# Kernel optimization log

Measured on AMD Instinct MI355X. Metric: run time of the kernel, lower is better.

The kernel has to match this reference:

```python
import math
import jax, jax.numpy as jnp
import numpy as np

N_HEADS = 16
D_EMBED = 1024
D_HEAD = D_EMBED // N_HEADS
BATCH = 2
SEQ = 2048


def setup_inputs() -> dict:
    key = jax.random.key(0)
    k1, k2, k3 = jax.random.split(key, 3)
    scale = 1.0 / math.sqrt(D_EMBED)
    return {
        "x": jax.random.normal(k1, (1, BATCH, SEQ, D_EMBED), dtype=jnp.float32),
        "w_in": jax.random.normal(k2, (3 * D_EMBED, D_EMBED), dtype=jnp.float32) * scale,
        "b_in": jnp.zeros((3 * D_EMBED,), dtype=jnp.float32),
        "w_out": jax.random.normal(k3, (D_EMBED, D_EMBED), dtype=jnp.float32) * scale,
        "b_out": jnp.zeros((D_EMBED,), dtype=jnp.float32),
        "causal_mask": 1,
    }


def reference(x, w_in, b_in, w_out, b_out, causal_mask):
    lead, B, S, D = x.shape  # lead == 1
    H, dh = N_HEADS, D_HEAD
    # fused QKV projection (torch Linear: x @ W^T + b)
    qkv = jnp.einsum("lbsd,ed->lbse", x, w_in) + b_in
    q, k, v = jnp.split(qkv, 3, axis=-1)
    # [1,B,S,D] -> [B,H,S,dh]
    def to_heads(t):
        return t.reshape(B, S, H, dh).transpose(0, 2, 1, 3)
    q, k, v = to_heads(q), to_heads(k), to_heads(v)
    # scaled dot-product attention with optional causal mask
    scores = jnp.einsum("bhqd,bhkd->bhqk", q, k)
    if causal_mask:
        mask = jnp.triu(jnp.ones((S, S), dtype=bool), k=1)
        scores = jnp.where(mask, -jnp.inf, scores)
    scores = scores / math.sqrt(dh)
    attn = jax.nn.softmax(scores, axis=-1)
    out = jnp.einsum("bhqk,bhkd->bhqd", attn, v)
    out = out.transpose(0, 2, 1, 3).reshape(lead, B, S, D)
    return jnp.einsum("lbsd,ed->lbse", out, w_out) + b_out
```

## Files before the change

kernel.cpp:

```cpp
#include <hip/hip_runtime.h>
#include <hip/hip_bf16.h>
#include <stdint.h>

#define S_LEN 2048
#define D_EMB 1024
#define NHEAD 16
#define DHEAD 64
#define NBATCH 2
#define MROWS 4096

typedef __attribute__((ext_vector_type(8))) short bf16x8;
typedef __attribute__((ext_vector_type(4))) float f32x4;
typedef unsigned short u16;
typedef unsigned int u32;

__device__ __forceinline__ u16 f2bf(float f) {
  union { float f; u32 u; } v; v.f = f;
  u32 r = v.u + 0x7fffu + ((v.u >> 16) & 1u);
  return (u16)(r >> 16);
}

__device__ __forceinline__ void gl_lds16(const void* g, void* l) {
  __builtin_amdgcn_global_load_lds(
      (const __attribute__((address_space(1))) u32*)g,
      (__attribute__((address_space(3))) u32*)l, 16, 0, 0);
}

__device__ __forceinline__ int swz(int o) { return o ^ (((o >> 7) & 7) << 4); }

__global__ void cast_f32_bf16(const float* __restrict__ in, u16* __restrict__ out, int n4) {
  int i = blockIdx.x * blockDim.x + threadIdx.x;
  if (i < n4) {
    float4 v = reinterpret_cast<const float4*>(in)[i];
    ushort4 o;
    o.x = f2bf(v.x); o.y = f2bf(v.y); o.z = f2bf(v.z); o.w = f2bf(v.w);
    reinterpret_cast<ushort4*>(out)[i] = o;
  }
}

template <int EPI>
__launch_bounds__(256, 2)
__global__ void gemm_bt(const u16* __restrict__ A, const u16* __restrict__ Bm,
                        const float* __restrict__ bias, int M, int N, int K,
                        u16* __restrict__ q_out, u16* __restrict__ k_out,
                        u16* __restrict__ vt_out, float* __restrict__ f_out) {
  __shared__ __align__(16) u16 As[2][128 * 32];
  __shared__ __align__(16) u16 Bs[2][128 * 32];
  const int t = threadIdx.x;
  const int w = t >> 6, lane = t & 63;
  const int m0 = blockIdx.y * 128, n0 = blockIdx.x * 128;
  const int wr = w >> 1, wc = w & 1;

  f32x4 acc[4][4] = {};

  const int e0 = w * 512 + lane * 8;
  const int ar0 = e0 >> 5, ac0 = e0 & 31;
  const int e1 = e0 + 2048;
  const int ar1 = e1 >> 5, ac1 = e1 & 31;
  const u16* Ab0 = A + (size_t)(m0 + ar0) * K + ac0;
  const u16* Ab1 = A + (size_t)(m0 + ar1) * K + ac1;
  const u16* Bb0 = Bm + (size_t)(n0 + ar0) * K + ac0;
  const u16* Bb1 = Bm + (size_t)(n0 + ar1) * K + ac1;

  const int lr = lane & 15, lg = lane >> 4;

#define GSTAGE(KT, BUF)                                \
  do {                                                 \
    gl_lds16(Ab0 + (KT), &As[BUF][w * 512]);           \
    gl_lds16(Ab1 + (KT), &As[BUF][w * 512 + 2048]);    \
    gl_lds16(Bb0 + (KT), &Bs[BUF][w * 512]);           \
    gl_lds16(Bb1 + (KT), &Bs[BUF][w * 512 + 2048]);    \
  } while (0)

  GSTAGE(0, 0);
  __syncthreads();
  int cur = 0;
  for (int kt = 0; kt < K; kt += 32) {
    if (kt + 32 < K) GSTAGE(kt + 32, cur ^ 1);
    bf16x8 af[4], bfr[4];
#pragma unroll
    for (int i = 0; i < 4; i++)
      af[i] = *(const bf16x8*)&As[cur][(wr * 64 + i * 16 + lr) * 32 + lg * 8];
#pragma unroll
    for (int j = 0; j < 4; j++)
      bfr[j] = *(const bf16x8*)&Bs[cur][(wc * 64 + j * 16 + lr) * 32 + lg * 8];
#pragma unroll
    for (int i = 0; i < 4; i++)
#pragma unroll
      for (int j = 0; j < 4; j++)
        acc[i][j] = __builtin_amdgcn_mfma_f32_16x16x32_bf16(af[i], bfr[j], acc[i][j], 0, 0, 0);
    __syncthreads();
    cur ^= 1;
  }
#undef GSTAGE

#pragma unroll
  for (int j = 0; j < 4; j++) {
    const int n = n0 + wc * 64 + j * 16 + lr;
    const float bv = bias[n];
#pragma unroll
    for (int i = 0; i < 4; i++) {
#pragma unroll
      for (int r = 0; r < 4; r++) {
        const int m = m0 + wr * 64 + i * 16 + lg * 4 + r;
        float v = acc[i][j][r] + bv;
        if (EPI == 0) {
          const int which = n >> 10, nn = n & 1023;
          const int h = nn >> 6, d = nn & 63;
          const int b = m >> 11, s = m & 2047;
          if (which == 0)
            q_out[(size_t)(((b * NHEAD + h) * S_LEN) + s) * DHEAD + d] = f2bf(v * 0.180336880f);
          else if (which == 1)
            k_out[(size_t)(((b * NHEAD + h) * S_LEN) + s) * DHEAD + d] = f2bf(v);
          else
            vt_out[(size_t)(((b * NHEAD + h) * DHEAD) + d) * S_LEN + s] = f2bf(v);
        } else {
          f_out[(size_t)m * N + n] = v;
        }
      }
    }
  }
}

__launch_bounds__(512, 2)
__global__ void attn_kernel(const u16* __restrict__ Qg, const u16* __restrict__ Kg,
                            const u16* __restrict__ Vtg, u16* __restrict__ AO,
                            const int* __restrict__ causal) {
  __shared__ __align__(16) u16 Kt[2][64 * 64];
  __shared__ __align__(16) u16 Vt[2][64 * 64];
  __shared__ __align__(16) u16 Pl[8][16 * 72];

  const int t = threadIdx.x, w = t >> 6, lane = t & 63;
  const int lr = lane & 15, lg = lane >> 4;
  const int nqt = (int)gridDim.x;
  const int qt = ((int)blockIdx.y < 16) ? (nqt - 1 - (int)blockIdx.x) : (int)blockIdx.x;
  const int bh = blockIdx.y;
  const size_t bh_off = (size_t)bh * S_LEN * DHEAD;
  const int cz = *causal;
  const int q0 = qt * 128;
  const int nk = cz ? (2 * qt + 2) : (S_LEN / 64);

  bf16x8 ones;
#pragma unroll
  for (int e = 0; e < 8; e++) ones[e] = (short)16256;

  {
    const char* qb = (const char*)(Qg + bh_off + (size_t)q0 * DHEAD);
#pragma unroll
    for (int c = 0; c < 2; c++) {
      int drel = c * 8192 + w * 1024 + lane * 16;
      gl_lds16(qb + swz(drel), (char*)&Kt[0][0] + c * 8192 + w * 1024);
    }
  }
  __syncthreads();
  bf16x8 qf[2];
#pragma unroll
  for (int ks = 0; ks < 2; ks++) {
    int rq = w * 16 + lr;
    qf[ks] = *(const bf16x8*)((const char*)&Kt[0][0] + swz(rq * 128 + ks * 64 + lg * 16));
  }
  __syncthreads();

  auto stageK = [&](int kt, int buf) {
    const char* kb = (const char*)(Kg + bh_off + (size_t)kt * 64 * DHEAD);
    int drel = w * 1024 + lane * 16;
    gl_lds16(kb + swz(drel), (char*)&Kt[buf][0] + w * 1024);
  };
  auto stageV = [&](int kt, int buf) {
    int drel = w * 1024 + lane * 16;
    int o = swz(drel);
    int row = o >> 7, colb = o & 127;
    const char* vb = (const char*)Vtg +
                     (((size_t)bh * DHEAD + row) * S_LEN + (size_t)kt * 64) * 2 + colb;
    gl_lds16(vb, (char*)&Vt[buf][0] + w * 1024);
  };

  float m_run[4], l_run[4];
  f32x4 o_acc[4] = {};
#pragma unroll
  for (int r = 0; r < 4; r++) { m_run[r] = -INFINITY; l_run[r] = 0.f; }

  stageK(0, 0);
  stageV(0, 0);
  __syncthreads();
  int cur = 0;

  for (int kt = 0; kt < nk; kt++) {
    if (kt + 1 < nk) {
      stageK(kt + 1, cur ^ 1);
      stageV(kt + 1, cur ^ 1);
    }

    f32x4 s[4] = {};
#pragma unroll
    for (int nf = 0; nf < 4; nf++) {
#pragma unroll
      for (int ks = 0; ks < 2; ks++) {
        int r = nf * 16 + lr;
        bf16x8 kf = *(const bf16x8*)((const char*)&Kt[cur][0] + swz(r * 128 + ks * 64 + lg * 16));
        s[nf] = __builtin_amdgcn_mfma_f32_16x16x32_bf16(qf[ks], kf, s[nf], 0, 0, 0);
      }
    }

    if (cz && (kt * 64 + 63 > q0 + w * 16)) {
#pragma unroll
      for (int nf = 0; nf < 4; nf++)
#pragma unroll
        for (int r = 0; r < 4; r++) {
          int kv = kt * 64 + nf * 16 + lr;
          int qr = q0 + w * 16 + lg * 4 + r;
          if (kv > qr) s[nf][r] = -INFINITY;
        }
    }

    float lmax[4];
#pragma unroll
    for (int r = 0; r < 4; r++)
      lmax[r] = fmaxf(fmaxf(s[0][r], s[1][r]), fmaxf(s[2][r], s[3][r]));
    float need = fmaxf(fmaxf(lmax[0] - m_run[0], lmax[1] - m_run[1]),
                       fmaxf(lmax[2] - m_run[2], lmax[3] - m_run[3]));
    if (!__all(need <= 8.0f)) {
      float rmax[4];
#pragma unroll
      for (int r = 0; r < 4; r++) rmax[r] = lmax[r];
#pragma unroll
      for (int mlt = 1; mlt < 16; mlt <<= 1)
#pragma unroll
        for (int r = 0; r < 4; r++) rmax[r] = fmaxf(rmax[r], __shfl_xor(rmax[r], mlt, 64));
#pragma unroll
      for (int r = 0; r < 4; r++) {
        float mn = fmaxf(m_run[r], rmax[r]);
        float scl = exp2f(m_run[r] - mn);
        m_run[r] = mn;
        l_run[r] *= scl;
#pragma unroll
        for (int nf = 0; nf < 4; nf++) o_acc[nf][r] *= scl;
      }
    }

#pragma unroll
    for (int nf = 0; nf < 4; nf++)
#pragma unroll
      for (int r = 0; r < 4; r++) {
        float p = exp2f(s[nf][r] - m_run[r]);
        Pl[w][(lg * 4 + r) * 72 + nf * 16 + lr] = f2bf(p);
      }

    asm volatile("s_waitcnt lgkmcnt(0)" ::: "memory");
    __builtin_amdgcn_sched_barrier(0);

    bf16x8 pf[2];
#pragma unroll
    for (int ks = 0; ks < 2; ks++)
      pf[ks] = *(const bf16x8*)&Pl[w][lr * 72 + ks * 32 + lg * 8];

    f32x4 lsum = {};
    lsum = __builtin_amdgcn_mfma_f32_16x16x32_bf16(pf[0], ones, lsum, 0, 0, 0);
    lsum = __builtin_amdgcn_mfma_f32_16x16x32_bf16(pf[1], ones, lsum, 0, 0, 0);

#pragma unroll
    for (int nf = 0; nf < 4; nf++) {
#pragma unroll
      for (int ks = 0; ks < 2; ks++) {
        int r = nf * 16 + lr;
        bf16x8 vf = *(const bf16x8*)((const char*)&Vt[cur][0] + swz(r * 128 + ks * 64 + lg * 16));
        o_acc[nf] = __builtin_amdgcn_mfma_f32_16x16x32_bf16(pf[ks], vf, o_acc[nf], 0, 0, 0);
      }
    }
#pragma unroll
    for (int r = 0; r < 4; r++) l_run[r] += lsum[r];

    __syncthreads();
    cur ^= 1;
  }

  const int b = bh >> 4, h = bh & 15;
#pragma unroll
  for (int nf = 0; nf < 4; nf++)
#pragma unroll
    for (int r = 0; r < 4; r++) {
      float v = o_acc[nf][r] / l_run[r];
      int qrow = q0 + w * 16 + lg * 4 + r;
      int d = nf * 16 + lr;
      AO[(size_t)(b * S_LEN + qrow) * D_EMB + h * DHEAD + d] = f2bf(v);
    }
}

extern "C" void kernel_launch(void* const* d_in, const int* in_sizes, int n_in,
                              void* d_out, int out_size, void* d_ws, size_t ws_size,
                              hipStream_t stream) {
  const float* x = (const float*)d_in[0];
  const float* w_in = (const float*)d_in[1];
  const float* b_in = (const float*)d_in[2];
  const float* w_out = (const float*)d_in[3];
  const float* b_out = (const float*)d_in[4];
  const int* causal = (const int*)d_in[5];
  float* out = (float*)d_out;

  char* p = (char*)d_ws;
  u16* xb = (u16*)p;  p += (size_t)MROWS * D_EMB * 2;
  u16* wib = (u16*)p; p += (size_t)3 * D_EMB * D_EMB * 2;
  u16* wob = (u16*)p; p += (size_t)D_EMB * D_EMB * 2;
  u16* Qg = (u16*)p;  p += (size_t)MROWS * D_EMB * 2;
  u16* Kg = (u16*)p;  p += (size_t)MROWS * D_EMB * 2;
  u16* Vtg = (u16*)p; p += (size_t)MROWS * D_EMB * 2;
  u16* AO = (u16*)p;  p += (size_t)MROWS * D_EMB * 2;

  {
    int n4 = MROWS * D_EMB / 4;
    cast_f32_bf16<<<(n4 + 255) / 256, 256, 0, stream>>>(x, xb, n4);
  }
  {
    int n4 = 3 * D_EMB * D_EMB / 4;
    cast_f32_bf16<<<(n4 + 255) / 256, 256, 0, stream>>>(w_in, wib, n4);
  }
  {
    int n4 = D_EMB * D_EMB / 4;
    cast_f32_bf16<<<(n4 + 255) / 256, 256, 0, stream>>>(w_out, wob, n4);
  }

  gemm_bt<0><<<dim3(3 * D_EMB / 128, MROWS / 128), 256, 0, stream>>>(
      xb, wib, b_in, MROWS, 3 * D_EMB, D_EMB, Qg, Kg, Vtg, nullptr);

  attn_kernel<<<dim3(S_LEN / 128, NBATCH * NHEAD), 512, 0, stream>>>(Qg, Kg, Vtg, AO, causal);

  gemm_bt<1><<<dim3(D_EMB / 128, MROWS / 128), 256, 0, stream>>>(
      AO, wob, b_out, MROWS, D_EMB, D_EMB, nullptr, nullptr, nullptr, out);
}
```

Baseline: 206.6 us.

## Use 256x256 tile GEMM with 512 threads for QKV projection

Replaces the templated 128x128 GEMM for the QKV projection with a dedicated kernel using 256x256 output tiles, a K-step of 64, 8 waves and swizzled LDS staging via direct global-to-LDS loads. This increases data reuse per LDS load and lowers the global traffic per FLOP. In exchange the grid shrinks to 192 blocks, which leaves some CUs idle, and the larger LDS and register footprint limits occupancy. The output projection keeps the old kernel, now specialised to fp32 output.

```diff
diff --git a/kernel.cpp b/kernel.cpp
--- a/kernel.cpp
+++ b/kernel.cpp
@@ -38,12 +38,91 @@
   }
 }
 
-template <int EPI>
+__launch_bounds__(512, 2)
+__global__ void gemm256_qkv(const u16* __restrict__ A, const u16* __restrict__ Bm,
+                            const float* __restrict__ bias,
+                            u16* __restrict__ q_out, u16* __restrict__ k_out,
+                            u16* __restrict__ vt_out) {
+  __shared__ __align__(16) u16 As[2][256 * 64];
+  __shared__ __align__(16) u16 Bs[2][256 * 64];
+  const int K = 1024;
+  const int t = threadIdx.x, w = t >> 6, lane = t & 63;
+  const int lr = lane & 15, lg = lane >> 4;
+  const int m0 = blockIdx.y * 256, n0 = blockIdx.x * 256;
+  const int wr = w >> 2, wc = w & 3;
+
+  f32x4 acc[8][4] = {};
+
+  const int srow = w * 8 + (lane >> 3);
+  const int scol = ((lane & 7) ^ (lane >> 3)) * 8;
+  const u16* Asrc = A + (size_t)(m0 + srow) * K + scol;
+  const u16* Bsrc = Bm + (size_t)(n0 + srow) * K + scol;
+
+#define STAGE256(KT, BUF)                                                     \
+  do {                                                                        \
+    _Pragma("unroll") for (int c = 0; c < 4; c++) {                           \
+      gl_lds16(Asrc + (size_t)(c * 64) * K + (KT), &As[BUF][c * 4096 + w * 512]); \
+      gl_lds16(Bsrc + (size_t)(c * 64) * K + (KT), &Bs[BUF][c * 4096 + w * 512]); \
+    }                                                                         \
+  } while (0)
+
+  const int xorv = (lane & 7) << 4;
+  const int ofk[2] = {(lg * 16) ^ xorv, (64 + lg * 16) ^ xorv};
+
+  STAGE256(0, 0);
+  __syncthreads();
+  int cur = 0;
+  for (int kt = 0; kt < K; kt += 64) {
+    if (kt + 64 < K) STAGE256(kt + 64, cur ^ 1);
+    const char* Ab = (const char*)&As[cur][0];
+    const char* Bb = (const char*)&Bs[cur][0];
+#pragma unroll
+    for (int ks = 0; ks < 2; ks++) {
+      bf16x8 bfr[4];
+#pragma unroll
+      for (int j = 0; j < 4; j++)
+        bfr[j] = *(const bf16x8*)(Bb + (wc * 64 + j * 16 + lr) * 128 + ofk[ks]);
+#pragma unroll
+      for (int i = 0; i < 8; i++) {
+        bf16x8 af = *(const bf16x8*)(Ab + (wr * 128 + i * 16 + lr) * 128 + ofk[ks]);
+#pragma unroll
+        for (int j = 0; j < 4; j++)
+          acc[i][j] = __builtin_amdgcn_mfma_f32_16x16x32_bf16(af, bfr[j], acc[i][j], 0, 0, 0);
+      }
+    }
+    __syncthreads();
+    cur ^= 1;
+  }
+#undef STAGE256
+
+#pragma unroll
+  for (int j = 0; j < 4; j++) {
+    const int n = n0 + wc * 64 + j * 16 + lr;
+    const float bv = bias[n];
+    const int which = n >> 10, nn = n & 1023;
+    const int h = nn >> 6, d = nn & 63;
+#pragma unroll
+    for (int i = 0; i < 8; i++) {
+#pragma unroll
+      for (int r = 0; r < 4; r++) {
+        const int m = m0 + wr * 128 + i * 16 + lg * 4 + r;
+        const int b = m >> 11, s = m & 2047;
+        float v = acc[i][j][r] + bv;
+        if (which == 0)
+          q_out[(size_t)(((b * NHEAD + h) * S_LEN) + s) * DHEAD + d] = f2bf(v * 0.180336880f);
+        else if (which == 1)
+          k_out[(size_t)(((b * NHEAD + h) * S_LEN) + s) * DHEAD + d] = f2bf(v);
+        else
+          vt_out[(size_t)(((b * NHEAD + h) * DHEAD) + d) * S_LEN + s] = f2bf(v);
+      }
+    }
+  }
+}
+
 __launch_bounds__(256, 2)
-__global__ void gemm_bt(const u16* __restrict__ A, const u16* __restrict__ Bm,
-                        const float* __restrict__ bias, int M, int N, int K,
-                        u16* __restrict__ q_out, u16* __restrict__ k_out,
-                        u16* __restrict__ vt_out, float* __restrict__ f_out) {
+__global__ void gemm_bt_f32(const u16* __restrict__ A, const u16* __restrict__ Bm,
+                            const float* __restrict__ bias, int M, int N, int K,
+                            float* __restrict__ f_out) {
   __shared__ __align__(16) u16 As[2][128 * 32];
   __shared__ __align__(16) u16 Bs[2][128 * 32];
   const int t = threadIdx.x;
@@ -103,20 +182,7 @@
 #pragma unroll
       for (int r = 0; r < 4; r++) {
         const int m = m0 + wr * 64 + i * 16 + lg * 4 + r;
-        float v = acc[i][j][r] + bv;
-        if (EPI == 0) {
-          const int which = n >> 10, nn = n & 1023;
-          const int h = nn >> 6, d = nn & 63;
-          const int b = m >> 11, s = m & 2047;
-          if (which == 0)
-            q_out[(size_t)(((b * NHEAD + h) * S_LEN) + s) * DHEAD + d] = f2bf(v * 0.180336880f);
-          else if (which == 1)
-            k_out[(size_t)(((b * NHEAD + h) * S_LEN) + s) * DHEAD + d] = f2bf(v);
-          else
-            vt_out[(size_t)(((b * NHEAD + h) * DHEAD) + d) * S_LEN + s] = f2bf(v);
-        } else {
-          f_out[(size_t)m * N + n] = v;
-        }
+        f_out[(size_t)m * N + n] = acc[i][j][r] + bv;
       }
     }
   }
@@ -319,11 +385,11 @@
     cast_f32_bf16<<<(n4 + 255) / 256, 256, 0, stream>>>(w_out, wob, n4);
   }
 
-  gemm_bt<0><<<dim3(3 * D_EMB / 128, MROWS / 128), 256, 0, stream>>>(
-      xb, wib, b_in, MROWS, 3 * D_EMB, D_EMB, Qg, Kg, Vtg, nullptr);
+  gemm256_qkv<<<dim3(3 * D_EMB / 256, MROWS / 256), 512, 0, stream>>>(
+      xb, wib, b_in, Qg, Kg, Vtg);
 
   attn_kernel<<<dim3(S_LEN / 128, NBATCH * NHEAD), 512, 0, stream>>>(Qg, Kg, Vtg, AO, causal);
 
-  gemm_bt<1><<<dim3(D_EMB / 128, MROWS / 128), 256, 0, stream>>>(
-      AO, wob, b_out, MROWS, D_EMB, D_EMB, nullptr, nullptr, nullptr, out);
-}
+  gemm_bt_f32<<<dim3(D_EMB / 128, MROWS / 128), 256, 0, stream>>>(
+      AO, wob, b_out, MROWS, D_EMB, D_EMB, out);
+}
```

After: 226.1 us. +9.5%, slower.

## Rewrite projection GEMMs with 4-stage LDS pipeline, swizzled tiles, and 8 warps

Applied to the files above, without the earlier changes.

Replaces the double-buffered K=32 GEMM with a 4-buffer K=64 pipeline that keeps three tile loads in flight, tracked by explicit vmcnt waits and a single barrier per iteration. LDS tiles are XOR-swizzled to avoid bank conflicts, and blocks grow to 512 threads, each wave computing a 64x32 sub-tile. The goal is to hide global-load latency and raise MFMA utilisation in both the QKV and output projections. The costs are 128KB of LDS per block, which limits occupancy, and K is now hardcoded to 1024.

```diff
diff --git a/kernel.cpp b/kernel.cpp
--- a/kernel.cpp
+++ b/kernel.cpp
@@ -39,65 +39,75 @@
 }
 
 template <int EPI>
-__launch_bounds__(256, 2)
-__global__ void gemm_bt(const u16* __restrict__ A, const u16* __restrict__ Bm,
-                        const float* __restrict__ bias, int M, int N, int K,
-                        u16* __restrict__ q_out, u16* __restrict__ k_out,
-                        u16* __restrict__ vt_out, float* __restrict__ f_out) {
-  __shared__ __align__(16) u16 As[2][128 * 32];
-  __shared__ __align__(16) u16 Bs[2][128 * 32];
-  const int t = threadIdx.x;
-  const int w = t >> 6, lane = t & 63;
+__launch_bounds__(512, 2)
+__global__ void gemm_pipe(const u16* __restrict__ A, const u16* __restrict__ Bm,
+                          const float* __restrict__ bias, int N,
+                          u16* __restrict__ q_out, u16* __restrict__ k_out,
+                          u16* __restrict__ vt_out, float* __restrict__ f_out) {
+  __shared__ __align__(16) u16 As[4][128 * 64];
+  __shared__ __align__(16) u16 Bs[4][128 * 64];
+  const int K = 1024, NT = 16;
+  const int t = threadIdx.x, w = t >> 6, lane = t & 63;
+  const int lr = lane & 15, lg = lane >> 4;
   const int m0 = blockIdx.y * 128, n0 = blockIdx.x * 128;
-  const int wr = w >> 1, wc = w & 1;
-
-  f32x4 acc[4][4] = {};
-
-  const int e0 = w * 512 + lane * 8;
-  const int ar0 = e0 >> 5, ac0 = e0 & 31;
-  const int e1 = e0 + 2048;
-  const int ar1 = e1 >> 5, ac1 = e1 & 31;
-  const u16* Ab0 = A + (size_t)(m0 + ar0) * K + ac0;
-  const u16* Ab1 = A + (size_t)(m0 + ar1) * K + ac1;
-  const u16* Bb0 = Bm + (size_t)(n0 + ar0) * K + ac0;
-  const u16* Bb1 = Bm + (size_t)(n0 + ar1) * K + ac1;
-
-  const int lr = lane & 15, lg = lane >> 4;
-
-#define GSTAGE(KT, BUF)                                \
-  do {                                                 \
-    gl_lds16(Ab0 + (KT), &As[BUF][w * 512]);           \
-    gl_lds16(Ab1 + (KT), &As[BUF][w * 512 + 2048]);    \
-    gl_lds16(Bb0 + (KT), &Bs[BUF][w * 512]);           \
-    gl_lds16(Bb1 + (KT), &Bs[BUF][w * 512 + 2048]);    \
+  const int wr = w >> 2, wc = w & 3;
+
+  f32x4 acc[4][2] = {};
+
+  const int srow = w * 8 + (lane >> 3);
+  const int scol = ((lane & 7) ^ (lane >> 3)) * 8;
+  const u16* Asrc = A + (size_t)(m0 + srow) * K + scol;
+  const u16* Bsrc = Bm + (size_t)(n0 + srow) * K + scol;
+
+#define STAGEP(T)                                                        \
+  do {                                                                   \
+    const int _kt = (T) * 64, _bf = (T) & 3;                             \
+    gl_lds16(Asrc + _kt, &As[_bf][w * 512]);                             \
+    gl_lds16(Asrc + (size_t)64 * K + _kt, &As[_bf][4096 + w * 512]);     \
+    gl_lds16(Bsrc + _kt, &Bs[_bf][w * 512]);                             \
+    gl_lds16(Bsrc + (size_t)64 * K + _kt, &Bs[_bf][4096 + w * 512]);     \
   } while (0)
 
-  GSTAGE(0, 0);
-  __syncthreads();
-  int cur = 0;
-  for (int kt = 0; kt < K; kt += 32) {
-    if (kt + 32 < K) GSTAGE(kt + 32, cur ^ 1);
-    bf16x8 af[4], bfr[4];
-#pragma unroll
-    for (int i = 0; i < 4; i++)
-      af[i] = *(const bf16x8*)&As[cur][(wr * 64 + i * 16 + lr) * 32 + lg * 8];
-#pragma unroll
-    for (int j = 0; j < 4; j++)
-      bfr[j] = *(const bf16x8*)&Bs[cur][(wc * 64 + j * 16 + lr) * 32 + lg * 8];
-#pragma unroll
-    for (int i = 0; i < 4; i++)
-#pragma unroll
-      for (int j = 0; j < 4; j++)
-        acc[i][j] = __builtin_amdgcn_mfma_f32_16x16x32_bf16(af[i], bfr[j], acc[i][j], 0, 0, 0);
-    __syncthreads();
-    cur ^= 1;
-  }
-#undef GSTAGE
-
-#pragma unroll
-  for (int j = 0; j < 4; j++) {
-    const int n = n0 + wc * 64 + j * 16 + lr;
+  const int xorv = (lane & 7) << 4;
+  const int ofk[2] = {(lg * 16) ^ xorv, (64 + lg * 16) ^ xorv};
+
+  STAGEP(0);
+  STAGEP(1);
+  STAGEP(2);
+
+  for (int kt = 0; kt < NT; kt++) {
+    if (kt < NT - 2)      asm volatile("s_waitcnt vmcnt(8)" ::: "memory");
+    else if (kt == NT - 2) asm volatile("s_waitcnt vmcnt(4)" ::: "memory");
+    else                   asm volatile("s_waitcnt vmcnt(0)" ::: "memory");
+    __builtin_amdgcn_s_barrier();
+
+    if (kt + 3 < NT) STAGEP(kt + 3);
+
+    const char* Ab = (const char*)&As[kt & 3][0];
+    const char* Bb = (const char*)&Bs[kt & 3][0];
+#pragma unroll
+    for (int ks = 0; ks < 2; ks++) {
+      bf16x8 bfr[2];
+#pragma unroll
+      for (int j = 0; j < 2; j++)
+        bfr[j] = *(const bf16x8*)(Bb + (wc * 32 + j * 16 + lr) * 128 + ofk[ks]);
+#pragma unroll
+      for (int i = 0; i < 4; i++) {
+        bf16x8 af = *(const bf16x8*)(Ab + (wr * 64 + i * 16 + lr) * 128 + ofk[ks]);
+#pragma unroll
+        for (int j = 0; j < 2; j++)
+          acc[i][j] = __builtin_amdgcn_mfma_f32_16x16x32_bf16(af, bfr[j], acc[i][j], 0, 0, 0);
+      }
+    }
+  }
+#undef STAGEP
+
+#pragma unroll
+  for (int j = 0; j < 2; j++) {
+    const int n = n0 + wc * 32 + j * 16 + lr;
     const float bv = bias[n];
+    const int which = n >> 10, nn = n & 1023;
+    const int h = nn >> 6, d = nn & 63;
 #pragma unroll
     for (int i = 0; i < 4; i++) {
 #pragma unroll
@@ -105,8 +115,6 @@
         const int m = m0 + wr * 64 + i * 16 + lg * 4 + r;
         float v = acc[i][j][r] + bv;
         if (EPI == 0) {
-          const int which = n >> 10, nn = n & 1023;
-          const int h = nn >> 6, d = nn & 63;
           const int b = m >> 11, s = m & 2047;
           if (which == 0)
             q_out[(size_t)(((b * NHEAD + h) * S_LEN) + s) * DHEAD + d] = f2bf(v * 0.180336880f);
@@ -319,11 +327,11 @@
     cast_f32_bf16<<<(n4 + 255) / 256, 256, 0, stream>>>(w_out, wob, n4);
   }
 
-  gemm_bt<0><<<dim3(3 * D_EMB / 128, MROWS / 128), 256, 0, stream>>>(
-      xb, wib, b_in, MROWS, 3 * D_EMB, D_EMB, Qg, Kg, Vtg, nullptr);
+  gemm_pipe<0><<<dim3(3 * D_EMB / 128, MROWS / 128), 512, 0, stream>>>(
+      xb, wib, b_in, 3 * D_EMB, Qg, Kg, Vtg, nullptr);
 
   attn_kernel<<<dim3(S_LEN / 128, NBATCH * NHEAD), 512, 0, stream>>>(Qg, Kg, Vtg, AO, causal);
 
-  gemm_bt<1><<<dim3(D_EMB / 128, MROWS / 128), 256, 0, stream>>>(
-      AO, wob, b_out, MROWS, D_EMB, D_EMB, nullptr, nullptr, nullptr, out);
-}
+  gemm_pipe<1><<<dim3(D_EMB / 128, MROWS / 128), 512, 0, stream>>>(
+      AO, wob, b_out, D_EMB, nullptr, nullptr, nullptr, out);
+}
```

Result: slower. 225.9 us (+9.3%).
